# Performance work log

Measured on AMD Instinct MI355X. Metric: run time of the kernel, lower is better.

Reference implementation:

```python
import jax, jax.numpy as jnp
import numpy as np

B, L, D = 8, 4096, 1024


def setup_inputs() -> dict:
    key = jax.random.key(0)
    k1, k2, k3 = jax.random.split(key, 3)
    scale = 1.0 / np.sqrt(D)  # ~xavier magnitude for DxD
    return {
        "x": jax.random.normal(k1, (B, L, D), dtype=jnp.float32),
        "hidden": jnp.zeros((B, D), dtype=jnp.float32),
        "Wg": jax.random.normal(k2, (D, D), dtype=jnp.float32) * scale,
        "bg": jnp.ones((D,), dtype=jnp.float32),  # gate bias init = 1.0
        "Wh": jax.random.normal(k3, (D, D), dtype=jnp.float32) * scale,
        "bh": jnp.zeros((D,), dtype=jnp.float32),
    }


def reference(x, hidden, Wg, bg, Wh, bh):
    # g_t = sigmoid(x W_g^T + b_g); c_t = tanh(x W_h^T + b_h)
    g = jax.nn.sigmoid(jnp.einsum('bld,ed->ble', x, Wg) + bg)
    c = jnp.tanh(jnp.einsum('bld,ed->ble', x, Wh) + bh)
    # linear recurrence h_t = a_t * h_{t-1} + b_t with a=g, b=(1-g)*c
    a = g
    b = (1.0 - g) * c

    def combine(left, right):
        al, bl = left
        ar, br = right
        return ar * al, ar * bl + br

    A, Bv = jax.lax.associative_scan(combine, (a, b), axis=1)
    # h_t = A_t * h0 + B_t  (cumulative affine map applied to init hidden)
    return A * hidden[:, None, :] + Bv
```

## Files before the change

kernel.cpp:

```cpp
#include <hip/hip_runtime.h>
#include <hip/hip_bf16.h>
#include <cstdint>


using u16   = unsigned short;
using f32x4 = __attribute__((ext_vector_type(4))) float;
using h16x4 = __attribute__((ext_vector_type(4))) _Float16;
using h16x8 = __attribute__((ext_vector_type(8))) _Float16;

#define M_TOTAL 32768
#define K_DIM   1024
#define E_DIM   1024
#define LCH     32
#define NCH     128

__global__ void conv_w(const float* __restrict__ wg, const float* __restrict__ wh,
                       u16* __restrict__ dst_base, int n4) {
    const float* w = blockIdx.y ? wh : wg;
    u16* dst = dst_base + (size_t)blockIdx.y * 1024 * 1024;
    int i = blockIdx.x * blockDim.x + threadIdx.x;
    if (i >= n4) return;
    f32x4 f = ((const f32x4*)w)[i];
    h16x4 h;
#pragma unroll
    for (int c = 0; c < 4; ++c) h[c] = (_Float16)f[c];
    ((h16x4*)dst)[i] = h;
}

__device__ inline float fast_sigmoid(float z) {
    return 1.f / (1.f + __expf(-z));
}
__device__ inline float fast_tanh(float z) {
    return 1.f - 2.f / (__expf(2.f * z) + 1.f);
}

__global__ __launch_bounds__(512, 4) void gemm_act(
    const float* __restrict__ x,
    const u16* __restrict__ wg_h, const u16* __restrict__ wh_h,
    const float* __restrict__ bg, const float* __restrict__ bh,
    _Float16* __restrict__ g_out, _Float16* __restrict__ c_out,
    float* __restrict__ Ac, float* __restrict__ Bc) {

    const int bid   = blockIdx.x;
    const int xcd   = bid & 7;
    const int local = bid >> 3;
    const int mt    = xcd * 32 + (local >> 3);
    const int et    = local & 7;
    const int e0    = et * 128;
    const int m0    = mt * 128;

    __shared__ __align__(16) union SM {
        struct {
            u16 A[128 * 40];
            u16 B[2][128 * 32];
        } s;
        struct {
            float g[32][132];
            float c[32][132];
        } ep;
    } sm;

    const int tid  = threadIdx.x;
    const int lane = tid & 63;
    const int wave = tid >> 6;
    const int wr = wave >> 2, wc = wave & 3;
    const int lr = lane & 15;
    const int kg = lane >> 4;

    const u16* __restrict__ Wptr[2] = {wg_h, wh_h};

    f32x4 accg[4][2], acch[4][2];
#pragma unroll
    for (int tr = 0; tr < 4; ++tr)
#pragma unroll
        for (int tc = 0; tc < 2; ++tc) {
            accg[tr][tc] = (f32x4){0.f, 0.f, 0.f, 0.f};
            acch[tr][tc] = (f32x4){0.f, 0.f, 0.f, 0.f};
        }

    for (int kt = 0; kt < K_DIM / 32; ++kt) {
        __syncthreads();

#pragma unroll
        for (int rgn = 0; rgn < 2; ++rgn) {
            int ch  = tid;
            int row = ch >> 2;
            int kq  = ch & 3;
            int kqs = kq ^ ((row >> 1) & 3);
            size_t goff = (size_t)(e0 + row) * K_DIM + kt * 32 + kqs * 8;
            __builtin_amdgcn_global_load_lds(
                (const __attribute__((address_space(1))) void*)(Wptr[rgn] + goff),
                (__attribute__((address_space(3))) void*)(&sm.s.B[rgn][ch * 8]), 16, 0, 0);
        }

#pragma unroll
        for (int j = 0; j < 2; ++j) {
            int q   = tid + 512 * j;
            int row = q >> 3;
            int kq  = q & 7;
            f32x4 f = *(const f32x4*)(x + (size_t)(m0 + row) * K_DIM + kt * 32 + kq * 4);
            h16x4 h;
#pragma unroll
            for (int c = 0; c < 4; ++c) h[c] = (_Float16)f[c];
            *(h16x4*)&sm.s.A[row * 40 + kq * 4] = h;
        }

        __syncthreads();

        h16x8 ah[4];
#pragma unroll
        for (int tr = 0; tr < 4; ++tr) {
            int r = wr * 64 + tr * 16 + lr;
            ah[tr] = *(const h16x8*)&sm.s.A[r * 40 + kg * 8];
        }
#pragma unroll
        for (int tc = 0; tc < 2; ++tc) {
            int e   = wc * 32 + tc * 16 + lr;
            int kgs = kg ^ ((e >> 1) & 3);
            h16x8 bgv = *(const h16x8*)&sm.s.B[0][e * 32 + kgs * 8];
            h16x8 bhv = *(const h16x8*)&sm.s.B[1][e * 32 + kgs * 8];
#pragma unroll
            for (int tr = 0; tr < 4; ++tr) {
                accg[tr][tc] = __builtin_amdgcn_mfma_f32_16x16x32_f16(ah[tr], bgv, accg[tr][tc], 0, 0, 0);
                acch[tr][tc] = __builtin_amdgcn_mfma_f32_16x16x32_f16(ah[tr], bhv, acch[tr][tc], 0, 0, 0);
            }
        }
    }

    float bgv[2], bhv[2];
#pragma unroll
    for (int tc = 0; tc < 2; ++tc) {
        int el = e0 + wc * 32 + tc * 16 + lr;
        bgv[tc] = bg[el];
        bhv[tc] = bh[el];
    }

#pragma unroll
    for (int s = 0; s < 4; ++s) {
        __syncthreads();
        if (wr == (s >> 1)) {
#pragma unroll
            for (int half = 0; half < 2; ++half) {
                int tr = (s & 1) * 2 + half;
#pragma unroll
                for (int tc = 0; tc < 2; ++tc) {
                    int el = wc * 32 + tc * 16 + lr;
#pragma unroll
                    for (int i = 0; i < 4; ++i) {
                        int row = half * 16 + kg * 4 + i;
                        sm.ep.g[row][el] = fast_sigmoid(accg[tr][tc][i] + bgv[tc]);
                        sm.ep.c[row][el] = fast_tanh(acch[tr][tc][i] + bhv[tc]);
                    }
                }
            }
        }
        __syncthreads();

        {
            int row = tid >> 4;
            int c8  = (tid & 15) * 8;
            size_t gofs = (size_t)(m0 + s * 32 + row) * E_DIM + e0 + c8;
            f32x4 v0 = *(const f32x4*)&sm.ep.g[row][c8];
            f32x4 v1 = *(const f32x4*)&sm.ep.g[row][c8 + 4];
            h16x8 hv;
#pragma unroll
            for (int j = 0; j < 4; ++j) { hv[j] = (_Float16)v0[j]; hv[j + 4] = (_Float16)v1[j]; }
            *(h16x8*)(g_out + gofs) = hv;
            v0 = *(const f32x4*)&sm.ep.c[row][c8];
            v1 = *(const f32x4*)&sm.ep.c[row][c8 + 4];
#pragma unroll
            for (int j = 0; j < 4; ++j) { hv[j] = (_Float16)v0[j]; hv[j + 4] = (_Float16)v1[j]; }
            *(h16x8*)(c_out + gofs) = hv;
        }

        if (tid < 128) {
            float A = 1.f, Bv = 0.f;
#pragma unroll 8
            for (int t = 0; t < LCH; ++t) {
                float g = (float)(_Float16)sm.ep.g[t][tid];
                float c = (float)(_Float16)sm.ep.c[t][tid];
                A  = g * A;
                Bv = g * Bv + (1.f - g) * c;
            }
            int m_abs = m0 + s * 32;
            int b  = m_abs >> 12;
            int ch = (m_abs & 4095) >> 5;
            size_t o = ((size_t)b * NCH + ch) * 1024 + e0 + tid;
            Ac[o] = A;
            Bc[o] = Bv;
        }
    }
}

__global__ void chunk_prefix(const float* __restrict__ Ac, const float* __restrict__ Bc,
                             const float* __restrict__ hidden, float* __restrict__ Hst) {
    int idx = blockIdx.x * 256 + threadIdx.x;
    int b = idx >> 10;
    int d = idx & 1023;
    float h = hidden[b * 1024 + d];
#pragma unroll 8
    for (int ch = 0; ch < NCH; ++ch) {
        size_t o = ((size_t)b * NCH + ch) * 1024 + d;
        float A = Ac[o], Bv = Bc[o];
        Hst[o] = h;
        h = A * h + Bv;
    }
}

__global__ void chunk_apply(const _Float16* __restrict__ g_arr,
                            const _Float16* __restrict__ c_arr,
                            const float* __restrict__ Hst,
                            float* __restrict__ out) {
    int d4 = threadIdx.x * 4;
    int ch = blockIdx.x;
    int b  = blockIdx.y;
    size_t base = ((size_t)b * 4096 + (size_t)ch * LCH) * 1024 + d4;
    size_t ho = ((size_t)b * NCH + ch) * 1024 + d4;
    f32x4 hv = *(const f32x4*)(Hst + ho);
    float h[4] = {hv[0], hv[1], hv[2], hv[3]};
#pragma unroll 4
    for (int t = 0; t < LCH; ++t) {
        size_t idx = base + (size_t)t * 1024;
        h16x4 gv = *(const h16x4*)(g_arr + idx);
        h16x4 cv = *(const h16x4*)(c_arr + idx);
#pragma unroll
        for (int j = 0; j < 4; ++j) {
            float g = (float)gv[j];
            float c = (float)cv[j];
            h[j] = g * h[j] + (1.f - g) * c;
        }
        *(f32x4*)(out + idx) = (f32x4){h[0], h[1], h[2], h[3]};
    }
}

extern "C" void kernel_launch(void* const* d_in, const int* in_sizes, int n_in,
                              void* d_out, int out_size, void* d_ws, size_t ws_size,
                              hipStream_t stream) {
    const float* x      = (const float*)d_in[0];
    const float* hidden = (const float*)d_in[1];
    const float* Wg     = (const float*)d_in[2];
    const float* bg     = (const float*)d_in[3];
    const float* Wh     = (const float*)d_in[4];
    const float* bh     = (const float*)d_in[5];
    float* out = (float*)d_out;

    char* ws = (char*)d_ws;
    const size_t WSEG = 2u * 1024u * 1024u;
    u16* wg_h = (u16*)(ws + 0 * WSEG);
    u16* wh_h = (u16*)(ws + 1 * WSEG);
    const size_t HBYTES = (size_t)M_TOTAL * E_DIM * 2;
    _Float16* g_arr = (_Float16*)(ws + 4 * WSEG);
    _Float16* c_arr = (_Float16*)(ws + 4 * WSEG + HBYTES);
    const size_t SSEG = (size_t)8 * NCH * 1024 * 4;
    float* Ac  = (float*)(ws + 4 * WSEG + 2 * HBYTES);
    float* Bc  = (float*)(ws + 4 * WSEG + 2 * HBYTES + SSEG);
    float* Hst = (float*)(ws + 4 * WSEG + 2 * HBYTES + 2 * SSEG);

    conv_w<<<dim3(1024, 2), 256, 0, stream>>>(Wg, Wh, wg_h, (1024 * 1024) / 4);

    gemm_act<<<dim3(2048), 512, 0, stream>>>(
        x, wg_h, wh_h, bg, bh, g_arr, c_arr, Ac, Bc);

    chunk_prefix<<<dim3(32), 256, 0, stream>>>(Ac, Bc, hidden, Hst);
    chunk_apply<<<dim3(NCH, 8), 256, 0, stream>>>(g_arr, c_arr, Hst, out);
}
```

Measured before the change: 529.0 us.

## Pre-convert x to fp16 and double-buffer GEMM tiles via direct global-to-LDS loads

A single prep kernel now converts x, Wg and Wh to fp16. The x copy is staged in the output buffer as scratch. The GEMM loads A and both B tiles with global_load_lds into a double-buffered, XOR-swizzled LDS layout, prefetching the next K tile while computing the current one and using one barrier per iteration. chunk_apply now handles 8 elements per thread with half the threads. The goal is to remove the per-tile in-register fp32-to-fp16 conversion and load stalls from the GEMM main loop, at the cost of an extra full pass over x to write and reread its fp16 copy.

```diff
diff --git a/kernel.cpp b/kernel.cpp
--- a/kernel.cpp
+++ b/kernel.cpp
@@ -14,17 +14,24 @@
 #define LCH     32
 #define NCH     128
 
-__global__ void conv_w(const float* __restrict__ wg, const float* __restrict__ wh,
-                       u16* __restrict__ dst_base, int n4) {
-    const float* w = blockIdx.y ? wh : wg;
-    u16* dst = dst_base + (size_t)blockIdx.y * 1024 * 1024;
-    int i = blockIdx.x * blockDim.x + threadIdx.x;
-    if (i >= n4) return;
-    f32x4 f = ((const f32x4*)w)[i];
+__global__ void prep(const float* __restrict__ x,
+                     const float* __restrict__ wg, const float* __restrict__ wh,
+                     u16* __restrict__ x16, u16* __restrict__ wg16,
+                     u16* __restrict__ wh16) {
+    const size_t XQ = (size_t)M_TOTAL * K_DIM / 4;
+    const size_t WQ = (size_t)K_DIM * E_DIM / 4;
+    size_t i = (size_t)blockIdx.x * 256 + threadIdx.x;
+    const float* src;
+    u16* dst;
+    size_t j;
+    if (i < XQ)           { src = x;  dst = x16;  j = i; }
+    else if (i < XQ + WQ) { src = wg; dst = wg16; j = i - XQ; }
+    else                  { src = wh; dst = wh16; j = i - XQ - WQ; }
+    f32x4 f = ((const f32x4*)src)[j];
     h16x4 h;
 #pragma unroll
     for (int c = 0; c < 4; ++c) h[c] = (_Float16)f[c];
-    ((h16x4*)dst)[i] = h;
+    ((h16x4*)dst)[j] = h;
 }
 
 __device__ inline float fast_sigmoid(float z) {
@@ -35,7 +42,7 @@
 }
 
 __global__ __launch_bounds__(512, 4) void gemm_act(
-    const float* __restrict__ x,
+    const u16* __restrict__ x16,
     const u16* __restrict__ wg_h, const u16* __restrict__ wh_h,
     const float* __restrict__ bg, const float* __restrict__ bh,
     _Float16* __restrict__ g_out, _Float16* __restrict__ c_out,
@@ -51,9 +58,9 @@
 
     __shared__ __align__(16) union SM {
         struct {
-            u16 A[128 * 40];
-            u16 B[2][128 * 32];
-        } s;
+            u16 A[512 * 8];
+            u16 B[2][512 * 8];
+        } buf[2];
         struct {
             float g[32][132];
             float c[32][132];
@@ -67,7 +74,30 @@
     const int lr = lane & 15;
     const int kg = lane >> 4;
 
-    const u16* __restrict__ Wptr[2] = {wg_h, wh_h};
+    const int sp   = tid >> 3;
+    const int sc   = tid & 7;
+    const int sclog = sc ^ (sp & 7);
+    const int srow  = sp * 2 + (sclog >> 2);
+    const int skc   = sclog & 3;
+    const u16* aSrc = x16 + (size_t)(m0 + srow) * K_DIM + skc * 8;
+    const u16* bgSrc = wg_h + (size_t)(e0 + srow) * K_DIM + skc * 8;
+    const u16* bhSrc = wh_h + (size_t)(e0 + srow) * K_DIM + skc * 8;
+
+    int aoff[4], boff[2];
+#pragma unroll
+    for (int tr = 0; tr < 4; ++tr) {
+        int r = wr * 64 + tr * 16 + lr;
+        int p = r >> 1;
+        int c = (((r & 1) << 2) | kg) ^ (p & 7);
+        aoff[tr] = p * 64 + c * 8;
+    }
+#pragma unroll
+    for (int tc = 0; tc < 2; ++tc) {
+        int e = wc * 32 + tc * 16 + lr;
+        int p = e >> 1;
+        int c = (((e & 1) << 2) | kg) ^ (p & 7);
+        boff[tc] = p * 64 + c * 8;
+    }
 
     f32x4 accg[4][2], acch[4][2];
 #pragma unroll
@@ -78,54 +108,53 @@
             acch[tr][tc] = (f32x4){0.f, 0.f, 0.f, 0.f};
         }
 
+#define STAGE(bi, kt)                                                          \
+    do {                                                                       \
+        size_t ko = (size_t)(kt) * 32;                                         \
+        __builtin_amdgcn_global_load_lds(                                      \
+            (const __attribute__((address_space(1))) void*)(aSrc + ko),        \
+            (__attribute__((address_space(3))) void*)(&sm.buf[bi].A[tid * 8]), \
+            16, 0, 0);                                                         \
+        __builtin_amdgcn_global_load_lds(                                      \
+            (const __attribute__((address_space(1))) void*)(bgSrc + ko),       \
+            (__attribute__((address_space(3))) void*)(&sm.buf[bi].B[0][tid * 8]),\
+            16, 0, 0);                                                         \
+        __builtin_amdgcn_global_load_lds(                                      \
+            (const __attribute__((address_space(1))) void*)(bhSrc + ko),       \
+            (__attribute__((address_space(3))) void*)(&sm.buf[bi].B[1][tid * 8]),\
+            16, 0, 0);                                                         \
+    } while (0)
+
+    STAGE(0, 0);
+    __syncthreads();
+
+    int cur = 0;
     for (int kt = 0; kt < K_DIM / 32; ++kt) {
-        __syncthreads();
-
-#pragma unroll
-        for (int rgn = 0; rgn < 2; ++rgn) {
-            int ch  = tid;
-            int row = ch >> 2;
-            int kq  = ch & 3;
-            int kqs = kq ^ ((row >> 1) & 3);
-            size_t goff = (size_t)(e0 + row) * K_DIM + kt * 32 + kqs * 8;
-            __builtin_amdgcn_global_load_lds(
-                (const __attribute__((address_space(1))) void*)(Wptr[rgn] + goff),
-                (__attribute__((address_space(3))) void*)(&sm.s.B[rgn][ch * 8]), 16, 0, 0);
-        }
-
-#pragma unroll
-        for (int j = 0; j < 2; ++j) {
-            int q   = tid + 512 * j;
-            int row = q >> 3;
-            int kq  = q & 7;
-            f32x4 f = *(const f32x4*)(x + (size_t)(m0 + row) * K_DIM + kt * 32 + kq * 4);
-            h16x4 h;
-#pragma unroll
-            for (int c = 0; c < 4; ++c) h[c] = (_Float16)f[c];
-            *(h16x4*)&sm.s.A[row * 40 + kq * 4] = h;
-        }
-
-        __syncthreads();
+        if (kt + 1 < K_DIM / 32) STAGE(cur ^ 1, kt + 1);
+
+        const u16* Ab  = sm.buf[cur].A;
+        const u16* Bg  = sm.buf[cur].B[0];
+        const u16* Bh  = sm.buf[cur].B[1];
 
         h16x8 ah[4];
 #pragma unroll
-        for (int tr = 0; tr < 4; ++tr) {
-            int r = wr * 64 + tr * 16 + lr;
-            ah[tr] = *(const h16x8*)&sm.s.A[r * 40 + kg * 8];
-        }
+        for (int tr = 0; tr < 4; ++tr)
+            ah[tr] = *(const h16x8*)&Ab[aoff[tr]];
 #pragma unroll
         for (int tc = 0; tc < 2; ++tc) {
-            int e   = wc * 32 + tc * 16 + lr;
-            int kgs = kg ^ ((e >> 1) & 3);
-            h16x8 bgv = *(const h16x8*)&sm.s.B[0][e * 32 + kgs * 8];
-            h16x8 bhv = *(const h16x8*)&sm.s.B[1][e * 32 + kgs * 8];
+            h16x8 bgv = *(const h16x8*)&Bg[boff[tc]];
+            h16x8 bhv = *(const h16x8*)&Bh[boff[tc]];
 #pragma unroll
             for (int tr = 0; tr < 4; ++tr) {
                 accg[tr][tc] = __builtin_amdgcn_mfma_f32_16x16x32_f16(ah[tr], bgv, accg[tr][tc], 0, 0, 0);
                 acch[tr][tc] = __builtin_amdgcn_mfma_f32_16x16x32_f16(ah[tr], bhv, acch[tr][tc], 0, 0, 0);
             }
         }
-    }
+
+        __syncthreads();
+        cur ^= 1;
+    }
+#undef STAGE
 
     float bgv[2], bhv[2];
 #pragma unroll
@@ -211,25 +240,27 @@
                             const _Float16* __restrict__ c_arr,
                             const float* __restrict__ Hst,
                             float* __restrict__ out) {
-    int d4 = threadIdx.x * 4;
+    int d8 = threadIdx.x * 8;
     int ch = blockIdx.x;
     int b  = blockIdx.y;
-    size_t base = ((size_t)b * 4096 + (size_t)ch * LCH) * 1024 + d4;
-    size_t ho = ((size_t)b * NCH + ch) * 1024 + d4;
-    f32x4 hv = *(const f32x4*)(Hst + ho);
-    float h[4] = {hv[0], hv[1], hv[2], hv[3]};
+    size_t base = ((size_t)b * 4096 + (size_t)ch * LCH) * 1024 + d8;
+    size_t ho = ((size_t)b * NCH + ch) * 1024 + d8;
+    f32x4 h0 = *(const f32x4*)(Hst + ho);
+    f32x4 h1 = *(const f32x4*)(Hst + ho + 4);
+    float h[8] = {h0[0], h0[1], h0[2], h0[3], h1[0], h1[1], h1[2], h1[3]};
 #pragma unroll 4
     for (int t = 0; t < LCH; ++t) {
         size_t idx = base + (size_t)t * 1024;
-        h16x4 gv = *(const h16x4*)(g_arr + idx);
-        h16x4 cv = *(const h16x4*)(c_arr + idx);
-#pragma unroll
-        for (int j = 0; j < 4; ++j) {
+        h16x8 gv = *(const h16x8*)(g_arr + idx);
+        h16x8 cv = *(const h16x8*)(c_arr + idx);
+#pragma unroll
+        for (int j = 0; j < 8; ++j) {
             float g = (float)gv[j];
             float c = (float)cv[j];
             h[j] = g * h[j] + (1.f - g) * c;
         }
-        *(f32x4*)(out + idx) = (f32x4){h[0], h[1], h[2], h[3]};
+        *(f32x4*)(out + idx)     = (f32x4){h[0], h[1], h[2], h[3]};
+        *(f32x4*)(out + idx + 4) = (f32x4){h[4], h[5], h[6], h[7]};
     }
 }
 
@@ -256,11 +287,15 @@
     float* Bc  = (float*)(ws + 4 * WSEG + 2 * HBYTES + SSEG);
     float* Hst = (float*)(ws + 4 * WSEG + 2 * HBYTES + 2 * SSEG);
 
-    conv_w<<<dim3(1024, 2), 256, 0, stream>>>(Wg, Wh, wg_h, (1024 * 1024) / 4);
+    u16* x16 = (u16*)d_out;
+
+    const int XQ = M_TOTAL * (K_DIM / 4);
+    const int WQ = K_DIM * (E_DIM / 4);
+    prep<<<dim3((XQ + 2 * WQ) / 256), 256, 0, stream>>>(x, Wg, Wh, x16, wg_h, wh_h);
 
     gemm_act<<<dim3(2048), 512, 0, stream>>>(
-        x, wg_h, wh_h, bg, bh, g_arr, c_arr, Ac, Bc);
+        x16, wg_h, wh_h, bg, bh, g_arr, c_arr, Ac, Bc);
 
     chunk_prefix<<<dim3(32), 256, 0, stream>>>(Ac, Bc, hidden, Hst);
-    chunk_apply<<<dim3(NCH, 8), 256, 0, stream>>>(g_arr, c_arr, Hst, out);
-}
+    chunk_apply<<<dim3(NCH, 8), 128, 0, stream>>>(g_arr, c_arr, Hst, out);
+}
```

New measurement: 458.1 us. 1.15x faster.
